# Performance work log

Hardware: AMD Instinct MI355X
Metric: run time of the kernel (lower is better)

## Reference

```python
import jax, jax.numpy as jnp
import numpy as np

FILTERS = 128

def setup_inputs() -> dict:
    key = jax.random.key(0)
    ks = jax.random.split(key, 8)
    B, Nq, Nkv, C = 4, 4096, 4096, 128
    q_inputs = jax.random.normal(ks[0], (B, Nq, C), dtype=jnp.float32)
    kv_inputs = jax.random.normal(ks[1], (B, Nkv, C), dtype=jnp.float32)
    s = 1.0 / np.sqrt(C)
    Wq = jax.random.normal(ks[2], (C, FILTERS), dtype=jnp.float32) * s
    Wk = jax.random.normal(ks[3], (C, FILTERS), dtype=jnp.float32) * s
    Wv = jax.random.normal(ks[4], (C, FILTERS), dtype=jnp.float32) * s
    bq = jnp.zeros((FILTERS,), jnp.float32)
    bk = jnp.zeros((FILTERS,), jnp.float32)
    bv = jnp.zeros((FILTERS,), jnp.float32)
    return {"q_inputs": q_inputs, "kv_inputs": kv_inputs,
            "Wq": Wq, "bq": bq, "Wk": Wk, "bk": bk, "Wv": Wv, "bv": bv}

def reference(q_inputs, kv_inputs, Wq, bq, Wk, bk, Wv, bv):
    # Dense projections (last-axis matmul + bias)
    q = jnp.einsum('bnc,cf->bnf', q_inputs, Wq) + bq
    k = jnp.einsum('bmc,cf->bmf', kv_inputs, Wk) + bk
    v = jnp.einsum('bmc,cf->bmf', kv_inputs, Wv) + bv
    scale = jnp.sqrt(jnp.asarray(FILTERS, jnp.float32))
    scores = jnp.einsum('bnf,bmf->bnm', q, k) / scale  # [B, Nq, Nkv]
    weights = jax.nn.softmax(scores, axis=-1)
    return jnp.einsum('bnm,bmf->bnf', weights, v)
```

## Files before the change

### kernel.cpp

```cpp
#include <hip/hip_runtime.h>
#include <stdint.h>

typedef unsigned short u16;
typedef unsigned int u32;
typedef __bf16 bf16x8 __attribute__((ext_vector_type(8)));
typedef unsigned short u16x8 __attribute__((ext_vector_type(8)));
typedef unsigned short u16x4 __attribute__((ext_vector_type(4)));
typedef float f32x4 __attribute__((ext_vector_type(4)));
typedef float f32x16 __attribute__((ext_vector_type(16)));

#define MFMA16(a, b, c) __builtin_amdgcn_mfma_f32_16x16x32_bf16((a), (b), (c), 0, 0, 0)
#define MFMA32(a, b, c) __builtin_amdgcn_mfma_f32_32x32x16_bf16((a), (b), (c), 0, 0, 0)

__device__ __forceinline__ u16 f2b(float f) {
    union { unsigned int i; float f; } v; v.f = f;
    unsigned int r = (v.i + 0x7FFFu + ((v.i >> 16) & 1u)) >> 16;
    return (u16)r;
}
__device__ __forceinline__ u32 pk2(float lo, float hi) {
    return (u32)f2b(lo) | ((u32)f2b(hi) << 16);
}
__device__ __forceinline__ void gload16(const void* g, void* l) {
    __builtin_amdgcn_global_load_lds(
        (const __attribute__((address_space(1))) u32*)g,
        (__attribute__((address_space(3))) u32*)l, 16, 0, 0);
}

constexpr int N = 4096;
constexpr int Cc = 128;
constexpr int Fc = 128;
constexpr int BATCH = 4;
constexpr int NT = N / 128;

constexpr int XS_STRIDE = 136;
constexpr int WT_STRIDE = 136;
constexpr int OM_STRIDE = 130;

__global__ __launch_bounds__(256) void wtrans_kernel(
    const float* __restrict__ Wq, const float* __restrict__ Wk,
    const float* __restrict__ Wv, u16* __restrict__ WtG)
{
    __shared__ __align__(16) u16 Wl[128 * 132];
    const int tid = threadIdx.x;
    const int which = blockIdx.x;
    const float* W = which == 0 ? Wq : (which == 1 ? Wk : Wv);
#pragma unroll
    for (int it = 0; it < 16; ++it) {
        int idx4 = tid + it * 256; int e0 = idx4 * 4;
        int c = e0 >> 7, f = e0 & 127;
        float4 wv = *(const float4*)(W + e0);
        u16x4 h; h[0] = f2b(wv.x); h[1] = f2b(wv.y); h[2] = f2b(wv.z); h[3] = f2b(wv.w);
        *(u16x4*)&Wl[c * 132 + f] = h;
    }
    __syncthreads();
    u16* out = WtG + which * 16384;
#pragma unroll
    for (int it = 0; it < 8; ++it) {
        int idx8 = tid + it * 256; int e0 = idx8 * 8;
        int f = e0 >> 7, c = e0 & 127;
        u16x8 h;
#pragma unroll
        for (int j = 0; j < 8; ++j) h[j] = Wl[(c + j) * 132 + f];
        *(u16x8*)(out + e0) = h;
    }
}

__global__ __launch_bounds__(256) void proj_kernel(
    const float* __restrict__ q_in, const float* __restrict__ kv_in,
    const u16* __restrict__ WtG,
    const float* __restrict__ bq, const float* __restrict__ bk,
    const float* __restrict__ bv,
    u16* __restrict__ Qw, u16* __restrict__ Kw, u16* __restrict__ Vtw)
{
    __shared__ __align__(16) u16 Xs[64 * XS_STRIDE];
    __shared__ __align__(16) u16 Wt[128 * WT_STRIDE];

    const int tid = threadIdx.x;
    const int which = blockIdx.y;
    const int b = blockIdx.z;
    const int m0 = blockIdx.x * 64;

    const float* X = (which == 0 ? q_in : kv_in) + ((size_t)b * N + m0) * Cc;
    const u16* Wsrc = WtG + which * 16384;
    const float* bias = which == 0 ? bq : (which == 1 ? bk : bv);

#pragma unroll
    for (int it = 0; it < 8; ++it) {
        int idx4 = tid + it * 256; int e0 = idx4 * 4;
        int r = e0 >> 7, c = e0 & 127;
        float4 xv = *(const float4*)(X + e0);
        u16x4 h; h[0] = f2b(xv.x); h[1] = f2b(xv.y); h[2] = f2b(xv.z); h[3] = f2b(xv.w);
        *(u16x4*)&Xs[r * XS_STRIDE + c] = h;
    }
#pragma unroll
    for (int it = 0; it < 8; ++it) {
        int idx8 = tid + it * 256; int e0 = idx8 * 8;
        int f = e0 >> 7, c = e0 & 127;
        *(u16x8*)&Wt[f * WT_STRIDE + c] = *(const u16x8*)(Wsrc + e0);
    }
    __syncthreads();

    const int lane = tid & 63;
    const int w = tid >> 6;
    const int n16 = lane & 15;
    const int quad = lane >> 4;

    if (which < 2) {
        bf16x8 ax[4];
#pragma unroll
        for (int kk = 0; kk < 4; ++kk)
            ax[kk] = *(const bf16x8*)&Xs[(w * 16 + n16) * XS_STRIDE + kk * 32 + quad * 8];
        const float scale = (which == 0) ? 0.08838834764831845f : 1.0f;
        const int swmask = (which == 1) ? 7 : 0;
        u16* Out = (which == 0) ? Qw : Kw;
#pragma unroll
        for (int ft = 0; ft < 8; ++ft) {
            f32x4 acc = {0.f, 0.f, 0.f, 0.f};
#pragma unroll
            for (int kk = 0; kk < 4; ++kk) {
                bf16x8 bw = *(const bf16x8*)&Wt[(ft * 16 + n16) * WT_STRIDE + kk * 32 + quad * 8];
                acc = MFMA16(ax[kk], bw, acc);
            }
            float bias_f = bias[ft * 16 + n16];
#pragma unroll
            for (int r = 0; r < 4; ++r) {
                int row = m0 + w * 16 + quad * 4 + r;
                int f = ft * 16 + n16;
                int fs = f ^ ((row & swmask) << 3);
                Out[((size_t)b * N + row) * Fc + fs] = f2b((acc[r] + bias_f) * scale);
            }
        }
    } else {
#pragma unroll
        for (int ft2 = 0; ft2 < 2; ++ft2) {
            int ftg = w * 2 + ft2;
            bf16x8 aw[4];
#pragma unroll
            for (int kk = 0; kk < 4; ++kk)
                aw[kk] = *(const bf16x8*)&Wt[(ftg * 16 + n16) * WT_STRIDE + kk * 32 + quad * 8];
            float bias4[4];
#pragma unroll
            for (int r = 0; r < 4; ++r) bias4[r] = bias[ftg * 16 + quad * 4 + r];
#pragma unroll
            for (int nt = 0; nt < 4; ++nt) {
                f32x4 acc = {0.f, 0.f, 0.f, 0.f};
#pragma unroll
                for (int kk = 0; kk < 4; ++kk) {
                    bf16x8 bx = *(const bf16x8*)&Xs[(nt * 16 + n16) * XS_STRIDE + kk * 32 + quad * 8];
                    acc = MFMA16(aw[kk], bx, acc);
                }
#pragma unroll
                for (int r = 0; r < 4; ++r) {
                    int fg = ftg * 16 + quad * 4 + r;
                    int rowg = m0 + nt * 16 + n16;
                    int rs = rowg ^ ((fg & 7) << 3);
                    Vtw[((size_t)b * Fc + fg) * N + rs] = f2b(acc[r] + bias4[r]);
                }
            }
        }
    }
}

__global__ __launch_bounds__(512, 2) void attn_kernel(
    const u16* __restrict__ Qw, const u16* __restrict__ Kw,
    const u16* __restrict__ Vtw, float* __restrict__ out)
{
    __shared__ __align__(16) char smem[134144];
    u16* const Ks0 = (u16*)smem;
    u16* const Ks1 = (u16*)(smem + 32768);
    u16* const Vs0 = (u16*)(smem + 65536);
    u16* const Vs1 = (u16*)(smem + 98304);

    const int tid = threadIdx.x;
    const int id = blockIdx.x + 64 * blockIdx.y;
    const int b = (id >> 1) & 3;
    const int q0 = (((id & 1) << 5) + (id >> 3)) << 6;

    const int lane = tid & 63;
    const int w = tid >> 6;
    const int kg = w & 3;
    const int qg = w >> 2;
    const int l31 = lane & 31;
    const int hi = lane >> 5;

    bf16x8 aq[8];
    {
        const u16* qp = Qw + ((size_t)b * N + q0 + qg * 32 + l31) * Cc + hi * 8;
#pragma unroll
        for (int kk = 0; kk < 8; ++kk) aq[kk] = *(const bf16x8*)(qp + kk * 16);
    }

    const u16* const Kb = Kw + (size_t)b * N * Cc;
    const u16* const Vb = Vtw + (size_t)b * Fc * N;

    const int rk = kg * 32 + l31;
    const int swk = (rk & 7) << 3;
    int koff[8];
#pragma unroll
    for (int kk = 0; kk < 8; ++kk)
        koff[kk] = rk * 128 + (((kk * 2 + hi) * 8) ^ swk);
    int voff[4][2];
#pragma unroll
    for (int cb = 0; cb < 4; ++cb) {
        int rv = cb * 32 + l31;
        int swv = (rv & 7) << 3;
#pragma unroll
        for (int ks = 0; ks < 2; ++ks)
            voff[cb][ks] = rv * 128 + (((kg * 4 + ks * 2 + hi) * 8) ^ swv);
    }

    f32x16 o[4];
#pragma unroll
    for (int cb = 0; cb < 4; ++cb)
#pragma unroll
        for (int i = 0; i < 16; ++i) o[cb][i] = 0.f;
    float lloc = 0.f;

    int ci[4];
#pragma unroll
    for (int it = 0; it < 4; ++it) ci[it] = tid + it * 512;

    auto STAGE = [&](u16* kd, u16* vd, int t) {
        const u16* ksrc = Kb + (size_t)t * (128 * 128);
        const u16* vsrc = Vb + t * 128;
#pragma unroll
        for (int it = 0; it < 4; ++it) {
            gload16(ksrc + ci[it] * 8, kd + ci[it] * 8);
            gload16(vsrc + (size_t)(ci[it] >> 4) * N + (ci[it] & 15) * 8, vd + ci[it] * 8);
        }
    };

    auto TILE_STEP = [&](const u16* Ksb, const u16* Vsb) {
        f32x16 st;
#pragma unroll
        for (int i = 0; i < 16; ++i) st[i] = 0.f;
#pragma unroll
        for (int kk = 0; kk < 8; ++kk) {
            bf16x8 ak = *(const bf16x8*)(Ksb + koff[kk]);
            st = MFMA32(ak, aq[kk], st);
        }
        float p[16];
#pragma unroll
        for (int i = 0; i < 16; ++i) p[i] = __expf(st[i]);
        lloc += ((((p[0] + p[1]) + (p[2] + p[3])) + ((p[4] + p[5]) + (p[6] + p[7])))
               + (((p[8] + p[9]) + (p[10] + p[11])) + ((p[12] + p[13]) + (p[14] + p[15]))));
        bf16x8 pb[2];
#pragma unroll
        for (int ks = 0; ks < 2; ++ks) {
            u32 a0 = pk2(p[ks * 8 + 0], p[ks * 8 + 1]);
            u32 a1 = pk2(p[ks * 8 + 2], p[ks * 8 + 3]);
            u32 a2 = pk2(p[ks * 8 + 4], p[ks * 8 + 5]);
            u32 a3 = pk2(p[ks * 8 + 6], p[ks * 8 + 7]);
            auto s02 = __builtin_amdgcn_permlane32_swap(a0, a2, false, false);
            auto s13 = __builtin_amdgcn_permlane32_swap(a1, a3, false, false);
            union { u32 u[4]; bf16x8 v; } bb;
            bb.u[0] = s02[0]; bb.u[1] = s13[0]; bb.u[2] = s02[1]; bb.u[3] = s13[1];
            pb[ks] = bb.v;
        }
#pragma unroll
        for (int cb = 0; cb < 4; ++cb) {
#pragma unroll
            for (int ks = 0; ks < 2; ++ks) {
                bf16x8 av = *(const bf16x8*)(Vsb + voff[cb][ks]);
                o[cb] = MFMA32(av, pb[ks], o[cb]);
            }
        }
    };

    STAGE(Ks0, Vs0, 0);
    __syncthreads();
    for (int t = 0; t < NT; t += 2) {
        if (t + 1 < NT) STAGE(Ks1, Vs1, t + 1);
        TILE_STEP(Ks0, Vs0);
        __syncthreads();
        if (t + 2 < NT) STAGE(Ks0, Vs0, t + 2);
        TILE_STEP(Ks1, Vs1);
        __syncthreads();
    }

    float lv = lloc + __shfl_xor(lloc, 32);

    float* const Om = (float*)smem;
    float* const Lm = (float*)(smem + 4 * 64 * OM_STRIDE * 4);

    const int qrow_w = qg * 32 + l31;
    const int crow0 = 4 * hi;
    {
        float* dst = Om + (size_t)(kg * 64 + qrow_w) * OM_STRIDE;
#pragma unroll
        for (int cb = 0; cb < 4; ++cb)
#pragma unroll
            for (int i = 0; i < 16; ++i) {
                int ch = cb * 32 + (i & 3) + 8 * (i >> 2) + crow0;
                dst[ch] = o[cb][i];
            }
        if (hi == 0) Lm[kg * 64 + qrow_w] = lv;
    }
    __syncthreads();

    const int qrow = tid >> 3;
    const int ch0 = (tid & 7) * 16;
    const float lsum = Lm[qrow] + Lm[64 + qrow] + Lm[128 + qrow] + Lm[192 + qrow];
    const float linv = 1.0f / lsum;
    float* op = out + ((size_t)b * N + q0 + qrow) * Fc + ch0;
#pragma unroll
    for (int j4 = 0; j4 < 4; ++j4) {
        f32x4 v;
#pragma unroll
        for (int jj = 0; jj < 4; ++jj) {
            int ch = ch0 + j4 * 4 + jj;
            float s = Om[(size_t)(0 * 64 + qrow) * OM_STRIDE + ch]
                    + Om[(size_t)(1 * 64 + qrow) * OM_STRIDE + ch]
                    + Om[(size_t)(2 * 64 + qrow) * OM_STRIDE + ch]
                    + Om[(size_t)(3 * 64 + qrow) * OM_STRIDE + ch];
            v[jj] = s * linv;
        }
        *(f32x4*)(op + j4 * 4) = v;
    }
}

extern "C" void kernel_launch(void* const* d_in, const int* in_sizes, int n_in,
                              void* d_out, int out_size, void* d_ws, size_t ws_size,
                              hipStream_t stream) {
    (void)in_sizes; (void)n_in; (void)out_size; (void)ws_size;
    const float* q_in  = (const float*)d_in[0];
    const float* kv_in = (const float*)d_in[1];
    const float* Wq = (const float*)d_in[2];
    const float* bq = (const float*)d_in[3];
    const float* Wk = (const float*)d_in[4];
    const float* bk = (const float*)d_in[5];
    const float* Wv = (const float*)d_in[6];
    const float* bv = (const float*)d_in[7];

    const size_t qkv = (size_t)BATCH * N * Fc;
    u16* Qw  = (u16*)d_ws;
    u16* Kw  = Qw + qkv;
    u16* Vtw = Kw + qkv;
    u16* WtG = Vtw + qkv;

    wtrans_kernel<<<dim3(3), dim3(256), 0, stream>>>(Wq, Wk, Wv, WtG);
    proj_kernel<<<dim3(64, 3, BATCH), dim3(256), 0, stream>>>(
        q_in, kv_in, WtG, bq, bk, bv, Qw, Kw, Vtw);
    attn_kernel<<<dim3(64, BATCH), dim3(512), 0, stream>>>(
        Qw, Kw, Vtw, (float*)d_out);
}
```

Baseline: 133.2 us.

## Load V directly into registers from global, use exp2 and packed bf16 convert

V tiles are no longer staged through LDS. Each wave gathers its V fragments straight from global memory into registers, prefetching the next tile after the PV MFMAs, and the V transpose swizzle is dropped. Q is prescaled by log2(e)/sqrt(F) so the softmax can use exp2f, the software bf16 rounding is replaced by the hardware v_cvt_pk_bf16_f32 instruction, and s_setprio is raised around the MFMA blocks. This removes LDS traffic and LDS space for V, but puts global-load latency on the critical path, and V bytes are fetched redundantly by waves that share a kv group.

```diff
diff --git a/kernel.cpp b/kernel.cpp
--- a/kernel.cpp
+++ b/kernel.cpp
@@ -1,5 +1,6 @@
 #include <hip/hip_runtime.h>
 #include <stdint.h>
+#include <math.h>
 
 typedef unsigned short u16;
 typedef unsigned int u32;
@@ -17,8 +18,9 @@
     unsigned int r = (v.i + 0x7FFFu + ((v.i >> 16) & 1u)) >> 16;
     return (u16)r;
 }
-__device__ __forceinline__ u32 pk2(float lo, float hi) {
-    return (u32)f2b(lo) | ((u32)f2b(hi) << 16);
+__device__ __forceinline__ u32 cvtpk(float lo, float hi) {
+    u32 r; asm("v_cvt_pk_bf16_f32 %0, %1, %2" : "=v"(r) : "v"(lo), "v"(hi));
+    return r;
 }
 __device__ __forceinline__ void gload16(const void* g, void* l) {
     __builtin_amdgcn_global_load_lds(
@@ -35,6 +37,8 @@
 constexpr int XS_STRIDE = 136;
 constexpr int WT_STRIDE = 136;
 constexpr int OM_STRIDE = 130;
+
+#define QSCALE 0.12751744750f
 
 __global__ __launch_bounds__(256) void wtrans_kernel(
     const float* __restrict__ Wq, const float* __restrict__ Wk,
@@ -110,7 +114,7 @@
 #pragma unroll
         for (int kk = 0; kk < 4; ++kk)
             ax[kk] = *(const bf16x8*)&Xs[(w * 16 + n16) * XS_STRIDE + kk * 32 + quad * 8];
-        const float scale = (which == 0) ? 0.08838834764831845f : 1.0f;
+        const float scale = (which == 0) ? QSCALE : 1.0f;
         const int swmask = (which == 1) ? 7 : 0;
         u16* Out = (which == 0) ? Qw : Kw;
 #pragma unroll
@@ -153,8 +157,7 @@
                 for (int r = 0; r < 4; ++r) {
                     int fg = ftg * 16 + quad * 4 + r;
                     int rowg = m0 + nt * 16 + n16;
-                    int rs = rowg ^ ((fg & 7) << 3);
-                    Vtw[((size_t)b * Fc + fg) * N + rs] = f2b(acc[r] + bias4[r]);
+                    Vtw[((size_t)b * Fc + fg) * N + rowg] = f2b(acc[r] + bias4[r]);
                 }
             }
         }
@@ -168,8 +171,6 @@
     __shared__ __align__(16) char smem[134144];
     u16* const Ks0 = (u16*)smem;
     u16* const Ks1 = (u16*)(smem + 32768);
-    u16* const Vs0 = (u16*)(smem + 65536);
-    u16* const Vs1 = (u16*)(smem + 98304);
 
     const int tid = threadIdx.x;
     const int id = blockIdx.x + 64 * blockIdx.y;
@@ -199,15 +200,6 @@
 #pragma unroll
     for (int kk = 0; kk < 8; ++kk)
         koff[kk] = rk * 128 + (((kk * 2 + hi) * 8) ^ swk);
-    int voff[4][2];
-#pragma unroll
-    for (int cb = 0; cb < 4; ++cb) {
-        int rv = cb * 32 + l31;
-        int swv = (rv & 7) << 3;
-#pragma unroll
-        for (int ks = 0; ks < 2; ++ks)
-            voff[cb][ks] = rv * 128 + (((kg * 4 + ks * 2 + hi) * 8) ^ swv);
-    }
 
     f32x16 o[4];
 #pragma unroll
@@ -220,61 +212,72 @@
 #pragma unroll
     for (int it = 0; it < 4; ++it) ci[it] = tid + it * 512;
 
-    auto STAGE = [&](u16* kd, u16* vd, int t) {
+    bf16x8 vr[8];
+    const u16* const vbase = Vb + (size_t)l31 * N + kg * 32 + hi * 8;
+
+    auto STAGE_K = [&](u16* kd, int t) {
         const u16* ksrc = Kb + (size_t)t * (128 * 128);
-        const u16* vsrc = Vb + t * 128;
-#pragma unroll
-        for (int it = 0; it < 4; ++it) {
+#pragma unroll
+        for (int it = 0; it < 4; ++it)
             gload16(ksrc + ci[it] * 8, kd + ci[it] * 8);
-            gload16(vsrc + (size_t)(ci[it] >> 4) * N + (ci[it] & 15) * 8, vd + ci[it] * 8);
-        }
     };
-
-    auto TILE_STEP = [&](const u16* Ksb, const u16* Vsb) {
+    auto GATHER_V = [&](int t) {
+        const u16* vp = vbase + t * 128;
+#pragma unroll
+        for (int cb = 0; cb < 4; ++cb)
+#pragma unroll
+            for (int ks = 0; ks < 2; ++ks)
+                vr[cb * 2 + ks] = *(const bf16x8*)(vp + (size_t)cb * 32 * N + ks * 16);
+    };
+
+    auto COMPUTE = [&](const u16* Ksb, int t) {
         f32x16 st;
 #pragma unroll
         for (int i = 0; i < 16; ++i) st[i] = 0.f;
+        __builtin_amdgcn_s_setprio(1);
 #pragma unroll
         for (int kk = 0; kk < 8; ++kk) {
             bf16x8 ak = *(const bf16x8*)(Ksb + koff[kk]);
             st = MFMA32(ak, aq[kk], st);
         }
+        __builtin_amdgcn_s_setprio(0);
         float p[16];
 #pragma unroll
-        for (int i = 0; i < 16; ++i) p[i] = __expf(st[i]);
+        for (int i = 0; i < 16; ++i) p[i] = exp2f(st[i]);
         lloc += ((((p[0] + p[1]) + (p[2] + p[3])) + ((p[4] + p[5]) + (p[6] + p[7])))
                + (((p[8] + p[9]) + (p[10] + p[11])) + ((p[12] + p[13]) + (p[14] + p[15]))));
         bf16x8 pb[2];
 #pragma unroll
         for (int ks = 0; ks < 2; ++ks) {
-            u32 a0 = pk2(p[ks * 8 + 0], p[ks * 8 + 1]);
-            u32 a1 = pk2(p[ks * 8 + 2], p[ks * 8 + 3]);
-            u32 a2 = pk2(p[ks * 8 + 4], p[ks * 8 + 5]);
-            u32 a3 = pk2(p[ks * 8 + 6], p[ks * 8 + 7]);
+            u32 a0 = cvtpk(p[ks * 8 + 0], p[ks * 8 + 1]);
+            u32 a1 = cvtpk(p[ks * 8 + 2], p[ks * 8 + 3]);
+            u32 a2 = cvtpk(p[ks * 8 + 4], p[ks * 8 + 5]);
+            u32 a3 = cvtpk(p[ks * 8 + 6], p[ks * 8 + 7]);
             auto s02 = __builtin_amdgcn_permlane32_swap(a0, a2, false, false);
             auto s13 = __builtin_amdgcn_permlane32_swap(a1, a3, false, false);
             union { u32 u[4]; bf16x8 v; } bb;
             bb.u[0] = s02[0]; bb.u[1] = s13[0]; bb.u[2] = s02[1]; bb.u[3] = s13[1];
             pb[ks] = bb.v;
         }
+        __builtin_amdgcn_s_setprio(1);
 #pragma unroll
         for (int cb = 0; cb < 4; ++cb) {
-#pragma unroll
-            for (int ks = 0; ks < 2; ++ks) {
-                bf16x8 av = *(const bf16x8*)(Vsb + voff[cb][ks]);
-                o[cb] = MFMA32(av, pb[ks], o[cb]);
-            }
-        }
+            o[cb] = MFMA32(vr[cb * 2 + 0], pb[0], o[cb]);
+            o[cb] = MFMA32(vr[cb * 2 + 1], pb[1], o[cb]);
+        }
+        __builtin_amdgcn_s_setprio(0);
+        if (t + 1 < NT) GATHER_V(t + 1);
     };
 
-    STAGE(Ks0, Vs0, 0);
+    STAGE_K(Ks0, 0);
+    GATHER_V(0);
     __syncthreads();
     for (int t = 0; t < NT; t += 2) {
-        if (t + 1 < NT) STAGE(Ks1, Vs1, t + 1);
-        TILE_STEP(Ks0, Vs0);
+        if (t + 1 < NT) STAGE_K(Ks1, t + 1);
+        COMPUTE(Ks0, t);
         __syncthreads();
-        if (t + 2 < NT) STAGE(Ks0, Vs0, t + 2);
-        TILE_STEP(Ks1, Vs1);
+        if (t + 2 < NT) STAGE_K(Ks0, t + 2);
+        COMPUTE(Ks1, t + 1);
         __syncthreads();
     }
 
```

Measured after the change: 179.8 us. 1.35x slower.
